# Optimization experiments

Hardware: AMD Instinct MI355X
Metric: run time of the kernel (lower is better)

Reference implementation:

```python
import jax, jax.numpy as jnp
import numpy as np

N = 50000       # nodes
E = 1600000     # edges (avg degree 32)
IN_DIM = 128
H_DIM = 128
OUT_DIM = 10
G = 512         # graphs in batch
K = 10          # APPNP propagation steps
ALPHA = 0.1


def _linear_params(key, fan_in, fan_out):
    kw, kb = jax.random.split(key)
    bound = 1.0 / np.sqrt(fan_in)
    W = jax.random.uniform(kw, (fan_in, fan_out), jnp.float32, -bound, bound)
    b = jax.random.uniform(kb, (fan_out,), jnp.float32, -bound, bound)
    return W, b


def setup_inputs() -> dict:
    key = jax.random.key(0)
    ks = jax.random.split(key, 8)
    features = jax.random.normal(ks[0], (IN_DIM, N), jnp.float32)
    edge_index = jax.random.randint(ks[1], (2, E), 0, N, jnp.int32)
    edge_weight = jax.random.uniform(ks[2], (E,), jnp.float32)
    batch = jnp.sort(jax.random.randint(ks[3], (N,), 0, G, jnp.int32))
    W1, b1 = _linear_params(ks[4], IN_DIM, H_DIM)
    W2, b2 = _linear_params(ks[5], H_DIM, H_DIM)
    V0w, V0b = _linear_params(ks[6], H_DIM, H_DIM)
    V1w, V1b = _linear_params(ks[7], H_DIM, OUT_DIM)
    return {"features": features, "edge_weight": edge_weight,
            "W1": W1, "b1": b1, "W2": W2, "b2": b2,
            "V0w": V0w, "V0b": V0b, "V1w": V1w, "V1b": V1b,
            "edge_index": edge_index, "batch": batch}


def reference(features, edge_weight, W1, b1, W2, b2, V0w, V0b, V1w, V1b,
              edge_index, batch):
    # features: [in_dim, N] -> nodes-first, matching `x = features.T`
    x = features.T @ W1 + b1          # [N, H]
    x = x @ W2 + b2                   # [N, H]

    src, dst = edge_index[0], edge_index[1]
    h = x  # teleport term
    # APPNP, normalize=False, dropout=0: x <- (1-a)*A_w x + a*h, K times
    for _ in range(K):
        msgs = edge_weight[:, None] * x[src]                  # [E, H]
        agg = jax.ops.segment_sum(msgs, dst, num_segments=N)  # [N, H]
        x = (1.0 - ALPHA) * agg + ALPHA * h

    pooled = jax.ops.segment_sum(x, batch, num_segments=G)    # [G, H]
    y = jax.nn.relu(pooled @ V0w + V0b)
    # dropout inactive in eval mode
    y = y @ V1w + V1b                                         # [G, OUT]
    return jax.nn.log_softmax(y, axis=1)
```

## Files before the change

kernel.cpp:

```cpp
#include <hip/hip_runtime.h>
#include <hip/hip_fp16.h>
#include <cstdint>

#define HD    128
#define OUTD  10
#define NG    512
#define KSTEPS 10

typedef unsigned short ushort_t;
typedef unsigned int   uint_t;

__device__ __forceinline__ float bf_lo(uint_t u) { return __uint_as_float(u << 16); }
__device__ __forceinline__ float bf_hi(uint_t u) { return __uint_as_float(u & 0xFFFF0000u); }
__device__ __forceinline__ uint_t f2bf_rne(float f) {
    uint_t u = __float_as_uint(f);
    return (u + 0x7FFFu + ((u >> 16) & 1u)) >> 16;
}
__device__ __forceinline__ uint_t pack_bf2(float lo, float hi) {
    return f2bf_rne(lo) | (f2bf_rne(hi) << 16);
}

__global__ void wc_kernel(const float* __restrict__ W1, const float* __restrict__ b1,
                          const float* __restrict__ W2, const float* __restrict__ b2,
                          float* __restrict__ Wc, float* __restrict__ bc) {
    int idx = blockIdx.x * 256 + threadIdx.x;
    int d = idx >> 7, j = idx & 127;
    float s = 0.f;
    for (int t = 0; t < HD; t++) s += W1[d * HD + t] * W2[t * HD + j];
    Wc[idx] = s;
    if (idx < HD) {
        float sb = b2[idx];
        for (int t = 0; t < HD; t++) sb += b1[t] * W2[t * HD + idx];
        bc[idx] = sb;
    }
}

__global__ void __launch_bounds__(256) feat_kernel(
        const float* __restrict__ feat, const float* __restrict__ Wc,
        const float* __restrict__ bc, ushort_t* __restrict__ h, int N) {
    __shared__ float ftile[HD][16];
    int tid = threadIdx.x;
    int n0 = blockIdx.x * 16;
    #pragma unroll
    for (int r = 0; r < 8; r++) {
        int l = tid * 8 + r;
        int d = l >> 4, n = l & 15;
        int nn = n0 + n;
        ftile[d][n] = (nn < N) ? feat[(size_t)d * N + nn] : 0.f;
    }
    __syncthreads();
    int j = tid & 127, half = tid >> 7;
    float acc[8];
    #pragma unroll
    for (int i = 0; i < 8; i++) acc[i] = 0.f;
    for (int d = 0; d < HD; d++) {
        float w = Wc[d * HD + j];
        #pragma unroll
        for (int i = 0; i < 8; i++) acc[i] += ftile[d][half * 8 + i] * w;
    }
    float bb = bc[j];
    #pragma unroll
    for (int i = 0; i < 8; i++) {
        int n = n0 + half * 8 + i;
        if (n < N) h[(size_t)n * HD + j] = (ushort_t)f2bf_rne(acc[i] + bb);
    }
}

__global__ void slot_kernel(const int* __restrict__ ei, int* __restrict__ cnt,
                            int* __restrict__ slot, int E) {
    int e = blockIdx.x * 256 + threadIdx.x;
    if (e < E) slot[e] = atomicAdd(&cnt[ei[E + e]], 1);
}

__global__ void scan1_kernel(const int* __restrict__ cnt, int* __restrict__ bsum, int N) {
    __shared__ int sm[4];
    int b = blockIdx.x, t = threadIdx.x, i = b * 256 + t;
    int v = (i < N) ? cnt[i] : 0;
    #pragma unroll
    for (int off = 32; off > 0; off >>= 1) v += __shfl_down(v, off);
    if ((t & 63) == 0) sm[t >> 6] = v;
    __syncthreads();
    if (t == 0) bsum[b] = sm[0] + sm[1] + sm[2] + sm[3];
}

__global__ void scan2_kernel(int* __restrict__ bsum, int nb) {
    __shared__ int sm[256];
    int t = threadIdx.x;
    int v = (t < nb) ? bsum[t] : 0;
    sm[t] = v;
    __syncthreads();
    for (int off = 1; off < 256; off <<= 1) {
        int u = (t >= off) ? sm[t - off] : 0;
        __syncthreads();
        sm[t] += u;
        __syncthreads();
    }
    if (t < nb) bsum[t] = sm[t] - v;
}

__global__ void scan3_kernel(const int* __restrict__ cnt, const int* __restrict__ bsum,
                             int* __restrict__ row_ptr, int N, int E) {
    __shared__ int sm[256];
    int b = blockIdx.x, t = threadIdx.x, i = b * 256 + t;
    int v = (i < N) ? cnt[i] : 0;
    sm[t] = v;
    __syncthreads();
    for (int off = 1; off < 256; off <<= 1) {
        int u = (t >= off) ? sm[t - off] : 0;
        __syncthreads();
        sm[t] += u;
        __syncthreads();
    }
    if (i < N) row_ptr[i] = bsum[b] + sm[t] - v;
    if (i == N) row_ptr[N] = E;
}

__global__ void place_kernel(const int* __restrict__ ei, const float* __restrict__ ew_in,
                             const int* __restrict__ slot, const int* __restrict__ row_ptr,
                             uint_t* __restrict__ erec, int E) {
    int e = blockIdx.x * 256 + threadIdx.x;
    if (e < E) {
        int d = ei[E + e];
        int p = row_ptr[d] + slot[e];
        uint_t r = ((uint_t)ei[e] << 16) |
                   (uint_t)__half_as_ushort(__float2half(ew_in[e]));
        __builtin_nontemporal_store(r, &erec[p]);
    }
}

__global__ void __launch_bounds__(256) prop_kernel(
        const ushort_t* __restrict__ xs, ushort_t* __restrict__ xd,
        const ushort_t* __restrict__ h, const int* __restrict__ row_ptr,
        const uint_t* __restrict__ erec, int N) {
    int wid = threadIdx.x >> 6, lane = threadIdx.x & 63;
    int node = blockIdx.x * 4 + wid;
    if (node >= N) return;
    int rs = row_ptr[node], re = row_ptr[node + 1];
    int grp = lane >> 4;
    int sub = lane & 15;

    float acc[8];
    #pragma unroll
    for (int i = 0; i < 8; i++) acc[i] = 0.f;

    uint_t p[8];
    #pragma unroll
    for (int u = 0; u < 8; u++) {
        int e = rs + grp + 4 * u;
        p[u] = (e < re) ? erec[e] : 0u;
    }

    for (int base = rs; base < re; base += 32) {
        uint_t q[8];
        #pragma unroll
        for (int u = 0; u < 8; u++) {
            int e = base + 32 + grp + 4 * u;
            q[u] = (e < re) ? erec[e] : 0u;
        }
        #pragma unroll
        for (int u = 0; u < 8; u++) {
            int   s = (int)(p[u] >> 16);
            float w = __half2float(__ushort_as_half((ushort_t)(p[u] & 0xFFFFu)));
            uint4 a = ((const uint4*)(xs + (size_t)s * HD))[sub];
            acc[0] += w * bf_lo(a.x); acc[1] += w * bf_hi(a.x);
            acc[2] += w * bf_lo(a.y); acc[3] += w * bf_hi(a.y);
            acc[4] += w * bf_lo(a.z); acc[5] += w * bf_hi(a.z);
            acc[6] += w * bf_lo(a.w); acc[7] += w * bf_hi(a.w);
        }
        #pragma unroll
        for (int u = 0; u < 8; u++) p[u] = q[u];
    }

    #pragma unroll
    for (int off = 32; off >= 16; off >>= 1) {
        #pragma unroll
        for (int i = 0; i < 8; i++) acc[i] += __shfl_down(acc[i], off);
    }

    if (grp == 0) {
        uint4 hv = ((const uint4*)(h + (size_t)node * HD))[sub];
        float hf[8];
        hf[0] = bf_lo(hv.x); hf[1] = bf_hi(hv.x);
        hf[2] = bf_lo(hv.y); hf[3] = bf_hi(hv.y);
        hf[4] = bf_lo(hv.z); hf[5] = bf_hi(hv.z);
        hf[6] = bf_lo(hv.w); hf[7] = bf_hi(hv.w);
        float o[8];
        #pragma unroll
        for (int i = 0; i < 8; i++) o[i] = 0.9f * acc[i] + 0.1f * hf[i];
        uint4 ov;
        ov.x = pack_bf2(o[0], o[1]);
        ov.y = pack_bf2(o[2], o[3]);
        ov.z = pack_bf2(o[4], o[5]);
        ov.w = pack_bf2(o[6], o[7]);
        ((uint4*)(xd + (size_t)node * HD))[sub] = ov;
    }
}

#define POOL_CHUNK 128
__global__ void pool_kernel(const ushort_t* __restrict__ x, const int* __restrict__ batch,
                            float* __restrict__ pooled, int N) {
    int j = threadIdx.x;
    int n0 = blockIdx.x * POOL_CHUNK;
    if (n0 >= N) return;
    int n1 = min(n0 + POOL_CHUNK, N);
    int cur = batch[n0];
    float acc = 0.f;
    for (int n = n0; n < n1; n++) {
        int g = batch[n];
        if (g != cur) {
            atomicAdd(&pooled[cur * HD + j], acc);
            acc = 0.f; cur = g;
        }
        acc += __uint_as_float(((uint_t)x[(size_t)n * HD + j]) << 16);
    }
    atomicAdd(&pooled[cur * HD + j], acc);
}

__global__ void head_kernel(const float* __restrict__ pooled, const float* __restrict__ V0w,
                            const float* __restrict__ V0b, const float* __restrict__ V1w,
                            const float* __restrict__ V1b, float* __restrict__ out) {
    __shared__ float prow[HD];
    __shared__ float y1[HD];
    __shared__ float y2[OUTD];
    __shared__ float lse;
    int g = blockIdx.x, j = threadIdx.x;
    prow[j] = pooled[g * HD + j];
    __syncthreads();
    float a = V0b[j];
    for (int d = 0; d < HD; d++) a += prow[d] * V0w[d * HD + j];
    y1[j] = a > 0.f ? a : 0.f;
    __syncthreads();
    if (j < OUTD) {
        float a2 = V1b[j];
        for (int t = 0; t < HD; t++) a2 += y1[t] * V1w[t * OUTD + j];
        y2[j] = a2;
    }
    __syncthreads();
    if (j == 0) {
        float m = y2[0];
        for (int o = 1; o < OUTD; o++) m = fmaxf(m, y2[o]);
        float s = 0.f;
        for (int o = 0; o < OUTD; o++) s += expf(y2[o] - m);
        lse = m + logf(s);
    }
    __syncthreads();
    if (j < OUTD) out[g * OUTD + j] = y2[j] - lse;
}

extern "C" void kernel_launch(void* const* d_in, const int* in_sizes, int n_in,
                              void* d_out, int out_size, void* d_ws, size_t ws_size,
                              hipStream_t stream) {
    const float* feat = (const float*)d_in[0];
    const float* ewt  = (const float*)d_in[1];
    const float* W1   = (const float*)d_in[2];
    const float* b1   = (const float*)d_in[3];
    const float* W2   = (const float*)d_in[4];
    const float* b2   = (const float*)d_in[5];
    const float* V0w  = (const float*)d_in[6];
    const float* V0b  = (const float*)d_in[7];
    const float* V1w  = (const float*)d_in[8];
    const float* V1b  = (const float*)d_in[9];
    const int*   ei   = (const int*)d_in[10];
    const int*   batch= (const int*)d_in[11];
    const int E = in_sizes[1];
    const int N = in_sizes[11];
    float* out = (float*)d_out;

    char* ws = (char*)d_ws;
    size_t off = 0;
    auto alloc = [&](size_t bytes) -> char* {
        char* p = ws + off;
        off = (off + bytes + 255) & ~(size_t)255;
        return p;
    };
    float*    Wc     = (float*)alloc((size_t)HD * HD * 4);
    float*    bc     = (float*)alloc((size_t)HD * 4);
    ushort_t* hb     = (ushort_t*)alloc((size_t)N * HD * 2);
    ushort_t* xA     = (ushort_t*)alloc((size_t)N * HD * 2);
    ushort_t* xB     = (ushort_t*)alloc((size_t)N * HD * 2);
    float*    pooled = (float*)alloc((size_t)NG * HD * 4);
    int*      row_ptr= (int*)alloc((size_t)(N + 1) * 4);
    int*      cnt    = (int*)alloc((size_t)N * 4);
    int*      bsum   = (int*)alloc((size_t)256 * 4);
    int*      slot   = (int*)alloc((size_t)E * 4);
    uint_t*   erec   = (uint_t*)alloc((size_t)E * 4);
    (void)ws_size;

    hipMemsetAsync(cnt, 0, (size_t)N * 4, stream);
    hipMemsetAsync(pooled, 0, (size_t)NG * HD * 4, stream);

    const int nb = (N + 255) / 256;

    wc_kernel<<<64, 256, 0, stream>>>(W1, b1, W2, b2, Wc, bc);
    feat_kernel<<<(N + 15) / 16, 256, 0, stream>>>(feat, Wc, bc, hb, N);
    slot_kernel<<<(E + 255) / 256, 256, 0, stream>>>(ei, cnt, slot, E);
    scan1_kernel<<<nb, 256, 0, stream>>>(cnt, bsum, N);
    scan2_kernel<<<1, 256, 0, stream>>>(bsum, nb);
    scan3_kernel<<<(N + 256) / 256, 256, 0, stream>>>(cnt, bsum, row_ptr, N, E);
    place_kernel<<<(E + 255) / 256, 256, 0, stream>>>(ei, ewt, slot, row_ptr, erec, E);

    const ushort_t* src = hb;
    ushort_t* dst = xA;
    for (int k = 0; k < KSTEPS; k++) {
        prop_kernel<<<(N + 3) / 4, 256, 0, stream>>>(src, dst, hb, row_ptr, erec, N);
        src = dst;
        dst = (dst == xA) ? xB : xA;
    }

    pool_kernel<<<(N + POOL_CHUNK - 1) / POOL_CHUNK, HD, 0, stream>>>(src, batch, pooled, N);
    head_kernel<<<NG, HD, 0, stream>>>(pooled, V0w, V0b, V1w, V1b, out);
}
```

Baseline: 803.5 us.

## Replace atomic CSR build with two-level bucket sort by destination

```diff
diff --git a/kernel.cpp b/kernel.cpp
--- a/kernel.cpp
+++ b/kernel.cpp
@@ -9,6 +9,7 @@
 
 typedef unsigned short ushort_t;
 typedef unsigned int   uint_t;
+typedef unsigned char  uchar_t;
 
 __device__ __forceinline__ float bf_lo(uint_t u) { return __uint_as_float(u << 16); }
 __device__ __forceinline__ float bf_hi(uint_t u) { return __uint_as_float(u & 0xFFFF0000u); }
@@ -66,27 +67,24 @@
     }
 }
 
-__global__ void slot_kernel(const int* __restrict__ ei, int* __restrict__ cnt,
-                            int* __restrict__ slot, int E) {
-    int e = blockIdx.x * 256 + threadIdx.x;
-    if (e < E) slot[e] = atomicAdd(&cnt[ei[E + e]], 1);
-}
-
-__global__ void scan1_kernel(const int* __restrict__ cnt, int* __restrict__ bsum, int N) {
-    __shared__ int sm[4];
-    int b = blockIdx.x, t = threadIdx.x, i = b * 256 + t;
-    int v = (i < N) ? cnt[i] : 0;
-    #pragma unroll
-    for (int off = 32; off > 0; off >>= 1) v += __shfl_down(v, off);
-    if ((t & 63) == 0) sm[t >> 6] = v;
-    __syncthreads();
-    if (t == 0) bsum[b] = sm[0] + sm[1] + sm[2] + sm[3];
-}
-
-__global__ void scan2_kernel(int* __restrict__ bsum, int nb) {
+
+__global__ void __launch_bounds__(256) bcount_kernel(
+        const int* __restrict__ ei, int* __restrict__ gbhist, int E, int chunk) {
+    __shared__ int lh[256];
+    int b = blockIdx.x, t = threadIdx.x;
+    lh[t] = 0;
+    __syncthreads();
+    int lo = b * chunk, hi = min(E, lo + chunk);
+    for (int i = lo + t; i < hi; i += 256) atomicAdd(&lh[ei[E + i] >> 8], 1);
+    __syncthreads();
+    if (lh[t]) atomicAdd(&gbhist[t], lh[t]);
+}
+
+__global__ void bscan_kernel(const int* __restrict__ gbhist, int* __restrict__ bucket_base,
+                             int* __restrict__ bcursor, int NBK, int E) {
     __shared__ int sm[256];
     int t = threadIdx.x;
-    int v = (t < nb) ? bsum[t] : 0;
+    int v = (t < NBK) ? gbhist[t] : 0;
     sm[t] = v;
     __syncthreads();
     for (int off = 1; off < 256; off <<= 1) {
@@ -95,36 +93,65 @@
         sm[t] += u;
         __syncthreads();
     }
-    if (t < nb) bsum[t] = sm[t] - v;
-}
-
-__global__ void scan3_kernel(const int* __restrict__ cnt, const int* __restrict__ bsum,
-                             int* __restrict__ row_ptr, int N, int E) {
-    __shared__ int sm[256];
-    int b = blockIdx.x, t = threadIdx.x, i = b * 256 + t;
-    int v = (i < N) ? cnt[i] : 0;
-    sm[t] = v;
+    int excl = sm[t] - v;
+    if (t < NBK) { bucket_base[t] = excl; bcursor[t] = excl; }
+    if (t == 0) bucket_base[NBK] = E;
+}
+
+__global__ void __launch_bounds__(256) bscatter_kernel(
+        const int* __restrict__ ei, const float* __restrict__ ewt,
+        int* __restrict__ bcursor, uint_t* __restrict__ rec_tmp,
+        uchar_t* __restrict__ dlo_tmp, int E, int chunk) {
+    __shared__ int lh[256];
+    __shared__ int lcur[256];
+    int b = blockIdx.x, t = threadIdx.x;
+    lh[t] = 0;
+    __syncthreads();
+    int lo = b * chunk, hi = min(E, lo + chunk);
+    for (int i = lo + t; i < hi; i += 256) atomicAdd(&lh[ei[E + i] >> 8], 1);
+    __syncthreads();
+    lcur[t] = lh[t] ? atomicAdd(&bcursor[t], lh[t]) : 0;
+    __syncthreads();
+    for (int i = lo + t; i < hi; i += 256) {
+        int d = ei[E + i];
+        int p = atomicAdd(&lcur[d >> 8], 1);
+        rec_tmp[p] = ((uint_t)ei[i] << 16) |
+                     (uint_t)__half_as_ushort(__float2half(ewt[i]));
+        dlo_tmp[p] = (uchar_t)(d & 255);
+    }
+}
+
+__global__ void __launch_bounds__(256) bsort_kernel(
+        const uint_t* __restrict__ rec_tmp, const uchar_t* __restrict__ dlo_tmp,
+        const int* __restrict__ bucket_base, int* __restrict__ row_ptr,
+        uint_t* __restrict__ erec, int N, int E) {
+    __shared__ int hist[256];
+    __shared__ int scn[256];
+    __shared__ int cur[256];
+    int b = blockIdx.x, t = threadIdx.x;
+    int lo = bucket_base[b], hi = bucket_base[b + 1];
+    hist[t] = 0;
+    __syncthreads();
+    for (int i = lo + t; i < hi; i += 256) atomicAdd(&hist[dlo_tmp[i]], 1);
+    __syncthreads();
+    int v = hist[t];
+    scn[t] = v;
     __syncthreads();
     for (int off = 1; off < 256; off <<= 1) {
-        int u = (t >= off) ? sm[t - off] : 0;
+        int u = (t >= off) ? scn[t - off] : 0;
         __syncthreads();
-        sm[t] += u;
+        scn[t] += u;
         __syncthreads();
     }
-    if (i < N) row_ptr[i] = bsum[b] + sm[t] - v;
-    if (i == N) row_ptr[N] = E;
-}
-
-__global__ void place_kernel(const int* __restrict__ ei, const float* __restrict__ ew_in,
-                             const int* __restrict__ slot, const int* __restrict__ row_ptr,
-                             uint_t* __restrict__ erec, int E) {
-    int e = blockIdx.x * 256 + threadIdx.x;
-    if (e < E) {
-        int d = ei[E + e];
-        int p = row_ptr[d] + slot[e];
-        uint_t r = ((uint_t)ei[e] << 16) |
-                   (uint_t)__half_as_ushort(__float2half(ew_in[e]));
-        __builtin_nontemporal_store(r, &erec[p]);
+    int excl = lo + scn[t] - v;
+    int node = (b << 8) + t;
+    if (node < N) row_ptr[node] = excl;
+    if (b == 0 && t == 0) row_ptr[N] = E;
+    cur[t] = excl;
+    __syncthreads();
+    for (int i = lo + t; i < hi; i += 256) {
+        int p = atomicAdd(&cur[dlo_tmp[i]], 1);
+        erec[p] = rec_tmp[i];
     }
 }
 
@@ -273,31 +300,34 @@
         off = (off + bytes + 255) & ~(size_t)255;
         return p;
     };
-    float*    Wc     = (float*)alloc((size_t)HD * HD * 4);
-    float*    bc     = (float*)alloc((size_t)HD * 4);
-    ushort_t* hb     = (ushort_t*)alloc((size_t)N * HD * 2);
-    ushort_t* xA     = (ushort_t*)alloc((size_t)N * HD * 2);
-    ushort_t* xB     = (ushort_t*)alloc((size_t)N * HD * 2);
-    float*    pooled = (float*)alloc((size_t)NG * HD * 4);
-    int*      row_ptr= (int*)alloc((size_t)(N + 1) * 4);
-    int*      cnt    = (int*)alloc((size_t)N * 4);
-    int*      bsum   = (int*)alloc((size_t)256 * 4);
-    int*      slot   = (int*)alloc((size_t)E * 4);
-    uint_t*   erec   = (uint_t*)alloc((size_t)E * 4);
+    float*    Wc        = (float*)alloc((size_t)HD * HD * 4);
+    float*    bc        = (float*)alloc((size_t)HD * 4);
+    ushort_t* hb        = (ushort_t*)alloc((size_t)N * HD * 2);
+    ushort_t* xA        = (ushort_t*)alloc((size_t)N * HD * 2);
+    ushort_t* xB        = (ushort_t*)alloc((size_t)N * HD * 2);
+    float*    pooled    = (float*)alloc((size_t)NG * HD * 4);
+    int*      row_ptr   = (int*)alloc((size_t)(N + 1) * 4);
+    int*      gbhist    = (int*)alloc((size_t)256 * 4);
+    int*      bucket_b  = (int*)alloc((size_t)257 * 4);
+    int*      bcursor   = (int*)alloc((size_t)256 * 4);
+    uint_t*   rec_tmp   = (uint_t*)alloc((size_t)E * 4);
+    uchar_t*  dlo_tmp   = (uchar_t*)alloc((size_t)E);
+    uint_t*   erec      = (uint_t*)alloc((size_t)E * 4);
     (void)ws_size;
 
-    hipMemsetAsync(cnt, 0, (size_t)N * 4, stream);
+    hipMemsetAsync(gbhist, 0, (size_t)256 * 4, stream);
     hipMemsetAsync(pooled, 0, (size_t)NG * HD * 4, stream);
 
-    const int nb = (N + 255) / 256;
+    const int NBK   = (N + 255) >> 8;
+    const int SBLK  = 256;
+    const int chunk = (E + SBLK - 1) / SBLK;
 
     wc_kernel<<<64, 256, 0, stream>>>(W1, b1, W2, b2, Wc, bc);
     feat_kernel<<<(N + 15) / 16, 256, 0, stream>>>(feat, Wc, bc, hb, N);
-    slot_kernel<<<(E + 255) / 256, 256, 0, stream>>>(ei, cnt, slot, E);
-    scan1_kernel<<<nb, 256, 0, stream>>>(cnt, bsum, N);
-    scan2_kernel<<<1, 256, 0, stream>>>(bsum, nb);
-    scan3_kernel<<<(N + 256) / 256, 256, 0, stream>>>(cnt, bsum, row_ptr, N, E);
-    place_kernel<<<(E + 255) / 256, 256, 0, stream>>>(ei, ewt, slot, row_ptr, erec, E);
+    bcount_kernel<<<SBLK, 256, 0, stream>>>(ei, gbhist, E, chunk);
+    bscan_kernel<<<1, 256, 0, stream>>>(gbhist, bucket_b, bcursor, NBK, E);
+    bscatter_kernel<<<SBLK, 256, 0, stream>>>(ei, ewt, bcursor, rec_tmp, dlo_tmp, E, chunk);
+    bsort_kernel<<<NBK, 256, 0, stream>>>(rec_tmp, dlo_tmp, bucket_b, row_ptr, erec, N, E);
 
     const ushort_t* src = hb;
     ushort_t* dst = xA;
```

Result: faster. 748.6 us (-6.8%).
